# Optimization experiments

Measured on AMD Instinct MI355X. Metric: run time of the kernel, lower is better.

## Reference

```python
import jax, jax.numpy as jnp
import numpy as np

B, T, D, H = 2, 2048, 1024, 16
HD = D // H  # 64
SCALE = 1.0 / np.sqrt(D).astype(np.float32)  # module uses 1/sqrt(mod_dim), not head_dim


def setup_inputs() -> dict:
    key = jax.random.key(0)
    k1, k2, k3 = jax.random.split(key, 3)
    x = jax.random.normal(k1, (B, T, D), dtype=jnp.float32)
    W_attn = jax.random.normal(k2, (3 * D, D), dtype=jnp.float32) * 0.02
    W_out = jax.random.normal(k3, (D, D), dtype=jnp.float32) * 0.02
    return {"x": x, "W_attn": W_attn, "W_out": W_out}


def reference(x, W_attn, W_out):
    b, t, d = x.shape
    # qkv projection (Linear, no bias): x @ W^T
    qkv = jnp.einsum('btd,ed->bte', x, W_attn)  # [b, t, 3d]
    q, k, v = jnp.split(qkv, 3, axis=-1)
    # [b, h, t, hd]
    q = q.reshape(b, t, H, HD).transpose(0, 2, 1, 3)
    k = k.reshape(b, t, H, HD).transpose(0, 2, 1, 3)
    v = v.reshape(b, t, H, HD).transpose(0, 2, 1, 3)
    # raw scores, causal mask applied before scaling (scale*-inf == -inf, so
    # equivalent to the original mask-then-scale order)
    att = jnp.einsum('bhqd,bhkd->bhqk', q, k)
    causal = jnp.tril(jnp.ones((t, t), dtype=bool))
    att = jnp.where(causal[None, None], att * SCALE, -jnp.inf)
    att = jax.nn.softmax(att, axis=-1)
    z = jnp.einsum('bhqk,bhkd->bhqd', att, v)
    z = z.transpose(0, 2, 1, 3).reshape(b, t, d)
    return jnp.einsum('btd,od->bto', z, W_out)
```

## Files before the change

### kernel.cpp

```cpp
#include <hip/hip_runtime.h>
#include <cstddef>

typedef unsigned short u16;
typedef __attribute__((ext_vector_type(4))) float floatx4;
typedef __attribute__((ext_vector_type(8))) short short8;
typedef __attribute__((ext_vector_type(4))) unsigned int uintx4;

#define TT 2048
#define DD 1024
#define NH 16
#define ATT_SCALE (1.0f / 32.0f)

__device__ __forceinline__ u16 f2bf(float f) {
  unsigned u = __builtin_bit_cast(unsigned, f);
  u += 0x7fffu + ((u >> 16) & 1u);
  return (u16)(u >> 16);
}

__device__ __forceinline__ unsigned pack2(float a, float b) {
#if __has_builtin(__builtin_amdgcn_cvt_pk_bf16_f32)
  auto t = __builtin_amdgcn_cvt_pk_bf16_f32(a, b);
  return __builtin_bit_cast(unsigned, t);
#else
  unsigned ua = __builtin_bit_cast(unsigned, a);
  ua += 0x7fffu + ((ua >> 16) & 1u);
  unsigned ub = __builtin_bit_cast(unsigned, b);
  ub += 0x7fffu + ((ub >> 16) & 1u);
  return (ua >> 16) | (ub & 0xffff0000u);
#endif
}

__device__ __forceinline__ void g2l16(const u16* g, u16* l) {
#if __has_builtin(__builtin_amdgcn_global_load_lds)
  __builtin_amdgcn_global_load_lds(
      (const __attribute__((address_space(1))) unsigned int*)g,
      (__attribute__((address_space(3))) unsigned int*)l, 16, 0, 0);
#else
  *(int4*)l = *(const int4*)g;
#endif
}

__device__ __forceinline__ short8 scale_q(short8 q) {
  short8 r;
#pragma unroll
  for (int i = 0; i < 8; ++i) {
    float f = __builtin_bit_cast(float, ((unsigned)(u16)q[i]) << 16) * ATT_SCALE;
    r[i] = (short)f2bf(f);
  }
  return r;
}

__global__ __launch_bounds__(256) void cvt3_kernel(const float* __restrict__ a,
                                                   const float* __restrict__ b,
                                                   const float* __restrict__ c,
                                                   u16* __restrict__ out,
                                                   int na, int nb, int nc) {
  int i = blockIdx.x * 256 + threadIdx.x;
  const float* src;
  int j;
  if (i < na) { src = a; j = i; }
  else if (i < na + nb) { src = b; j = i - na; }
  else if (i < na + nb + nc) { src = c; j = i - na - nb; }
  else return;
  float4 v = ((const float4*)src)[j];
  ((ushort4*)out)[i] = make_ushort4(f2bf(v.x), f2bf(v.y), f2bf(v.z), f2bf(v.w));
}

template <int MODE, int BN>
__global__ __launch_bounds__(256) void gemm_bt(const u16* __restrict__ A,
                                               const u16* __restrict__ Bm,
                                               void* __restrict__ C,
                                               u16* __restrict__ vt,
                                               int M, int N, int K) {
  constexpr int NT = BN / 32;
  __shared__ u16 As[128 * 32];
  __shared__ u16 Bs[BN * 32];
  const int tid = threadIdx.x;
  const int lane = tid & 63;
  const int wave = tid >> 6;
  const int quad = lane >> 4;
  const int l16 = lane & 15;
  const int wm = (wave >> 1) * 64;
  const int wn = (wave & 1) * (BN / 2);
  const int m0 = blockIdx.x * 128;
  const int n0 = blockIdx.y * BN;

  const int srow = wave * 16 + (lane >> 2);
  const int scol = (lane & 3) * 8;
  const int sl = wave * 512 + lane * 8;

  floatx4 acc[4][NT] = {};

  for (int k0 = 0; k0 < K; k0 += 32) {
    __syncthreads();
    g2l16(&A[(size_t)(m0 + srow) * K + k0 + scol], &As[sl]);
    g2l16(&A[(size_t)(m0 + 64 + srow) * K + k0 + scol], &As[2048 + sl]);
    g2l16(&Bm[(size_t)(n0 + srow) * K + k0 + scol], &Bs[sl]);
    if (BN == 128)
      g2l16(&Bm[(size_t)(n0 + 64 + srow) * K + k0 + scol], &Bs[2048 + sl]);
    __syncthreads();

    short8 af[4];
#pragma unroll
    for (int mt = 0; mt < 4; ++mt)
      af[mt] = *(const short8*)&As[(wm + mt * 16 + l16) * 32 + quad * 8];
#pragma unroll
    for (int nt = 0; nt < NT; ++nt) {
      short8 bf = *(const short8*)&Bs[(wn + nt * 16 + l16) * 32 + quad * 8];
#pragma unroll
      for (int mt = 0; mt < 4; ++mt)
        acc[mt][nt] = __builtin_amdgcn_mfma_f32_16x16x32_bf16(af[mt], bf, acc[mt][nt], 0, 0, 0);
    }
  }

  if (MODE == 2 && n0 >= 2048) {
    const int bidx = m0 >> 11;
    const int tbase = (m0 & 2047) + wm;
#pragma unroll
    for (int mt = 0; mt < 4; ++mt)
#pragma unroll
      for (int nt = 0; nt < NT; ++nt) {
        int gn = n0 + wn + nt * 16 + l16;
        size_t vrow = (size_t)(bidx * 1024 + gn - 2048);
        int t = tbase + mt * 16 + quad * 4;
        uint2 val;
        val.x = pack2(acc[mt][nt][0], acc[mt][nt][1]);
        val.y = pack2(acc[mt][nt][2], acc[mt][nt][3]);
        *(uint2*)&vt[vrow * TT + t] = val;
      }
  } else {
    const int cw = (MODE == 2) ? 2048 : N;
#pragma unroll
    for (int mt = 0; mt < 4; ++mt)
#pragma unroll
      for (int nt = 0; nt < NT; ++nt)
#pragma unroll
        for (int r = 0; r < 4; ++r) {
          int gm = m0 + wm + mt * 16 + quad * 4 + r;
          int gn = n0 + wn + nt * 16 + l16;
          float v = acc[mt][nt][r];
          if (MODE >= 1)
            ((u16*)C)[(size_t)gm * cw + gn] = f2bf(v);
          else
            ((float*)C)[(size_t)gm * cw + gn] = v;
        }
  }
}

template <bool DIAG>
__device__ __forceinline__ void exp_pack(const floatx4* s, int kt0, int quad,
                                         int qr, float& ps, unsigned W[4][2]) {
#pragma unroll
  for (int nt = 0; nt < 4; ++nt) {
    float e[4];
#pragma unroll
    for (int r = 0; r < 4; ++r) {
      float v = __expf(s[nt][r]);
      if (DIAG) {
        int kk = kt0 + nt * 16 + quad * 4 + r;
        v = (kk <= qr) ? v : 0.f;
      }
      ps += v;
      e[r] = v;
    }
    W[nt][0] = pack2(e[0], e[1]);
    W[nt][1] = pack2(e[2], e[3]);
  }
}

__device__ __forceinline__ void pfrag(const unsigned W[4][2], int bpA, int bpB,
                                      int quad, short8& pa0, short8& pa1) {
  uintx4 a, b;
#pragma unroll
  for (int c = 0; c < 2; ++c) {
    unsigned x0 = (unsigned)__builtin_amdgcn_ds_bpermute(bpA, (int)W[0][c]);
    unsigned x1 = (unsigned)__builtin_amdgcn_ds_bpermute(bpA, (int)W[1][c]);
    unsigned y0 = (unsigned)__builtin_amdgcn_ds_bpermute(bpB, (int)W[0][c]);
    unsigned y1 = (unsigned)__builtin_amdgcn_ds_bpermute(bpB, (int)W[1][c]);
    a[c]     = (quad < 2) ? x0 : x1;
    a[2 + c] = (quad < 2) ? y0 : y1;
    unsigned u0 = (unsigned)__builtin_amdgcn_ds_bpermute(bpA, (int)W[2][c]);
    unsigned u1 = (unsigned)__builtin_amdgcn_ds_bpermute(bpA, (int)W[3][c]);
    unsigned t0 = (unsigned)__builtin_amdgcn_ds_bpermute(bpB, (int)W[2][c]);
    unsigned t1 = (unsigned)__builtin_amdgcn_ds_bpermute(bpB, (int)W[3][c]);
    b[c]     = (quad < 2) ? u0 : u1;
    b[2 + c] = (quad < 2) ? t0 : t1;
  }
  pa0 = __builtin_bit_cast(short8, a);
  pa1 = __builtin_bit_cast(short8, b);
}

__global__ __launch_bounds__(512, 4) void attn_flash6(const u16* __restrict__ qk,
                                                      const u16* __restrict__ vt,
                                                      u16* __restrict__ z) {
  __shared__ u16 Ks[2][64 * 64];
  __shared__ u16 Vs[2][64 * 64];

  const int tid = threadIdx.x;
  const int lane = tid & 63;
  const int wave = tid >> 6;
  const int qs = wave & 3;
  const int par = wave >> 2;
  const int quad = lane >> 4;
  const int l16 = lane & 15;

  const int p = blockIdx.x;
  const int qtA = p, qtB = 31 - p;
  const int bh = blockIdx.y;
  const int b = bh >> 4, h = bh & 15;

  const size_t bbase = (size_t)b * TT * 2048;
  const u16* qg = qk + bbase + h * 64;
  const u16* kg = qk + bbase + 1024 + h * 64;
  const u16* vtg = vt + (size_t)bh * 64 * TT;

  short8 qfA[2], qfB[2];
  {
    const size_t ra = (size_t)(qtA * 64 + qs * 16 + l16) * 2048;
    const size_t rb = (size_t)(qtB * 64 + qs * 16 + l16) * 2048;
    qfA[0] = scale_q(*(const short8*)&qg[ra + quad * 8]);
    qfA[1] = scale_q(*(const short8*)&qg[ra + 32 + quad * 8]);
    qfB[0] = scale_q(*(const short8*)&qg[rb + quad * 8]);
    qfB[1] = scale_q(*(const short8*)&qg[rb + 32 + quad * 8]);
  }

  floatx4 OA[4] = {}, OB[4] = {};
  float psA = 0.f, psB = 0.f;

  const int tsel = tid >> 8;
  const int t8 = tid & 255;
  const int str = t8 >> 2, sc = (t8 & 3) * 16;
  const int swr = (str & 7) << 3;

  const int nktB = qtB + 1;
  const int M = (nktB + 1) >> 1;
  const int qrA = qtA * 64 + qs * 16 + l16;
  const int qrB = qtB * 64 + qs * 16 + l16;

  const int sw = (l16 & 7) << 3;
  const int rc0 = (quad * 8) ^ sw;
  const int rc1 = (32 + quad * 8) ^ sw;
  const int bpA = ((((lane >> 4) & 1) << 5) | l16) << 2;
  const int bpB = bpA + 64;

  for (int m = 0; m < M; ++m) {
    const int kt = 2 * m + par;
    const int kt0 = kt * 64;
    __syncthreads();
    {
      const int kst = 2 * m + tsel;
      if (kst < nktB) {
        *(int4*)&Ks[tsel][str * 64 + (sc ^ swr)] =
            *(const int4*)&kg[(size_t)(kst * 64 + str) * 2048 + sc];
        *(int4*)&Ks[tsel][str * 64 + ((sc + 8) ^ swr)] =
            *(const int4*)&kg[(size_t)(kst * 64 + str) * 2048 + sc + 8];
        *(int4*)&Vs[tsel][str * 64 + (sc ^ swr)] =
            *(const int4*)&vtg[(size_t)str * TT + kst * 64 + sc];
        *(int4*)&Vs[tsel][str * 64 + ((sc + 8) ^ swr)] =
            *(const int4*)&vtg[(size_t)str * TT + kst * 64 + sc + 8];
      }
    }
    __syncthreads();

    if (kt < nktB) {
      floatx4 s[4];
      __builtin_amdgcn_s_setprio(1);
#pragma unroll
      for (int nt = 0; nt < 4; ++nt) {
        const int ro = (nt * 16 + l16) * 64;
        short8 k0 = *(const short8*)&Ks[par][ro + rc0];
        short8 k1 = *(const short8*)&Ks[par][ro + rc1];
        floatx4 zz = {0.f, 0.f, 0.f, 0.f};
        s[nt] = __builtin_amdgcn_mfma_f32_16x16x32_bf16(k0, qfB[0], zz, 0, 0, 0);
        s[nt] = __builtin_amdgcn_mfma_f32_16x16x32_bf16(k1, qfB[1], s[nt], 0, 0, 0);
      }
      __builtin_amdgcn_s_setprio(0);
      short8 pa0, pa1;
      {
        unsigned W[4][2];
        if (kt == qtB)
          exp_pack<true>(s, kt0, quad, qrB, psB, W);
        else
          exp_pack<false>(s, kt0, quad, qrB, psB, W);
        pfrag(W, bpA, bpB, quad, pa0, pa1);
      }
      __builtin_amdgcn_s_setprio(1);
#pragma unroll
      for (int nt = 0; nt < 4; ++nt) {
        const int ro = (nt * 16 + l16) * 64;
        short8 v0 = *(const short8*)&Vs[par][ro + rc0];
        short8 v1 = *(const short8*)&Vs[par][ro + rc1];
        OB[nt] = __builtin_amdgcn_mfma_f32_16x16x32_bf16(pa0, v0, OB[nt], 0, 0, 0);
        OB[nt] = __builtin_amdgcn_mfma_f32_16x16x32_bf16(pa1, v1, OB[nt], 0, 0, 0);
      }
      __builtin_amdgcn_s_setprio(0);

      if (kt <= qtA) {
        __builtin_amdgcn_s_setprio(1);
#pragma unroll
        for (int nt = 0; nt < 4; ++nt) {
          const int ro = (nt * 16 + l16) * 64;
          short8 k0 = *(const short8*)&Ks[par][ro + rc0];
          short8 k1 = *(const short8*)&Ks[par][ro + rc1];
          floatx4 zz = {0.f, 0.f, 0.f, 0.f};
          s[nt] = __builtin_amdgcn_mfma_f32_16x16x32_bf16(k0, qfA[0], zz, 0, 0, 0);
          s[nt] = __builtin_amdgcn_mfma_f32_16x16x32_bf16(k1, qfA[1], s[nt], 0, 0, 0);
        }
        __builtin_amdgcn_s_setprio(0);
        {
          unsigned W[4][2];
          if (kt == qtA)
            exp_pack<true>(s, kt0, quad, qrA, psA, W);
          else
            exp_pack<false>(s, kt0, quad, qrA, psA, W);
          pfrag(W, bpA, bpB, quad, pa0, pa1);
        }
        __builtin_amdgcn_s_setprio(1);
#pragma unroll
        for (int nt = 0; nt < 4; ++nt) {
          const int ro = (nt * 16 + l16) * 64;
          short8 v0 = *(const short8*)&Vs[par][ro + rc0];
          short8 v1 = *(const short8*)&Vs[par][ro + rc1];
          OA[nt] = __builtin_amdgcn_mfma_f32_16x16x32_bf16(pa0, v0, OA[nt], 0, 0, 0);
          OA[nt] = __builtin_amdgcn_mfma_f32_16x16x32_bf16(pa1, v1, OA[nt], 0, 0, 0);
        }
        __builtin_amdgcn_s_setprio(0);
      }
    }
  }

  psA += __shfl_xor(psA, 16);
  psA += __shfl_xor(psA, 32);
  psB += __shfl_xor(psB, 16);
  psB += __shfl_xor(psB, 32);

  float* red = (float*)Ks;
  float* lred = (float*)Vs;

  __syncthreads();
  if (par == 1) {
#pragma unroll
    for (int nt = 0; nt < 4; ++nt)
#pragma unroll
      for (int r = 0; r < 4; ++r)
        red[(qs * 16 + quad * 4 + r) * 64 + nt * 16 + l16] = OA[nt][r];
  }
  if (quad == 0) lred[par * 64 + qs * 16 + l16] = psA;
  __syncthreads();
  if (par == 0) {
#pragma unroll
    for (int r = 0; r < 4; ++r) {
      int row = qs * 16 + quad * 4 + r;
      float rl = 1.0f / (lred[row] + lred[64 + row]);
      int qa = qtA * 64 + row;
#pragma unroll
      for (int nt = 0; nt < 4; ++nt) {
        float o = OA[nt][r] + red[row * 64 + nt * 16 + l16];
        z[(size_t)(b * TT + qa) * DD + h * 64 + nt * 16 + l16] = f2bf(o * rl);
      }
    }
  }
  __syncthreads();
  if (par == 1) {
#pragma unroll
    for (int nt = 0; nt < 4; ++nt)
#pragma unroll
      for (int r = 0; r < 4; ++r)
        red[(qs * 16 + quad * 4 + r) * 64 + nt * 16 + l16] = OB[nt][r];
  }
  if (quad == 0) lred[par * 64 + qs * 16 + l16] = psB;
  __syncthreads();
  if (par == 0) {
#pragma unroll
    for (int r = 0; r < 4; ++r) {
      int row = qs * 16 + quad * 4 + r;
      float rl = 1.0f / (lred[row] + lred[64 + row]);
      int qb = qtB * 64 + row;
#pragma unroll
      for (int nt = 0; nt < 4; ++nt) {
        float o = OB[nt][r] + red[row * 64 + nt * 16 + l16];
        z[(size_t)(b * TT + qb) * DD + h * 64 + nt * 16 + l16] = f2bf(o * rl);
      }
    }
  }
}

extern "C" void kernel_launch(void* const* d_in, const int* in_sizes, int n_in,
                              void* d_out, int out_size, void* d_ws, size_t ws_size,
                              hipStream_t stream) {
  const float* x  = (const float*)d_in[0];
  const float* Wa = (const float*)d_in[1];
  const float* Wo = (const float*)d_in[2];
  float* out = (float*)d_out;

  u16* xb  = (u16*)d_ws;
  u16* Wab = xb  + (size_t)4096 * 1024;
  u16* Wob = Wab + (size_t)3072 * 1024;
  u16* qk  = Wob + (size_t)1024 * 1024;
  u16* z   = qk  + (size_t)4096 * 2048;
  u16* vt  = z   + (size_t)4096 * 1024;

  cvt3_kernel<<<8192, 256, 0, stream>>>(x, Wa, Wo, xb, 1048576, 786432, 262144);

  gemm_bt<2, 128><<<dim3(32, 24), 256, 0, stream>>>(xb, Wab, qk, vt, 4096, 3072, 1024);

  attn_flash6<<<dim3(16, 2 * NH), 512, 0, stream>>>(qk, vt, z);

  gemm_bt<0, 64><<<dim3(32, 16), 256, 0, stream>>>(z, Wob, out, nullptr, 4096, 1024, 1024);
}
```

Baseline: 180.0 us.

## Replace paired causal query tiles with one tile per block, heaviest first

The attention kernel no longer pairs query tile p with tile 31-p in one block for causal load balancing. Each block now handles a single query tile, launched in descending order so the longest tiles start first, doubling the grid to 32x32 blocks. Launch bounds rise to 8 blocks per CU to fit more resident blocks. This cuts per-block register use and gives finer scheduling granularity, but each K/V tile loaded into shared memory now serves only one query tile, and the extra blocks repeat setup and K/V loads.

```diff
diff --git a/kernel.cpp b/kernel.cpp
--- a/kernel.cpp
+++ b/kernel.cpp
@@ -190,7 +190,7 @@
   pa1 = __builtin_bit_cast(short8, b);
 }
 
-__global__ __launch_bounds__(512, 4) void attn_flash6(const u16* __restrict__ qk,
+__global__ __launch_bounds__(512, 8) void attn_flash7(const u16* __restrict__ qk,
                                                       const u16* __restrict__ vt,
                                                       u16* __restrict__ z) {
   __shared__ u16 Ks[2][64 * 64];
@@ -204,8 +204,7 @@
   const int quad = lane >> 4;
   const int l16 = lane & 15;
 
-  const int p = blockIdx.x;
-  const int qtA = p, qtB = 31 - p;
+  const int qt = 31 - blockIdx.x;
   const int bh = blockIdx.y;
   const int b = bh >> 4, h = bh & 15;
 
@@ -214,28 +213,24 @@
   const u16* kg = qk + bbase + 1024 + h * 64;
   const u16* vtg = vt + (size_t)bh * 64 * TT;
 
-  short8 qfA[2], qfB[2];
+  short8 qf[2];
   {
-    const size_t ra = (size_t)(qtA * 64 + qs * 16 + l16) * 2048;
-    const size_t rb = (size_t)(qtB * 64 + qs * 16 + l16) * 2048;
-    qfA[0] = scale_q(*(const short8*)&qg[ra + quad * 8]);
-    qfA[1] = scale_q(*(const short8*)&qg[ra + 32 + quad * 8]);
-    qfB[0] = scale_q(*(const short8*)&qg[rb + quad * 8]);
-    qfB[1] = scale_q(*(const short8*)&qg[rb + 32 + quad * 8]);
-  }
-
-  floatx4 OA[4] = {}, OB[4] = {};
-  float psA = 0.f, psB = 0.f;
+    const size_t ra = (size_t)(qt * 64 + qs * 16 + l16) * 2048;
+    qf[0] = scale_q(*(const short8*)&qg[ra + quad * 8]);
+    qf[1] = scale_q(*(const short8*)&qg[ra + 32 + quad * 8]);
+  }
+
+  floatx4 O[4] = {};
+  float ps = 0.f;
 
   const int tsel = tid >> 8;
   const int t8 = tid & 255;
   const int str = t8 >> 2, sc = (t8 & 3) * 16;
   const int swr = (str & 7) << 3;
 
-  const int nktB = qtB + 1;
-  const int M = (nktB + 1) >> 1;
-  const int qrA = qtA * 64 + qs * 16 + l16;
-  const int qrB = qtB * 64 + qs * 16 + l16;
+  const int nkt = qt + 1;
+  const int M = (nkt + 1) >> 1;
+  const int qr = qt * 64 + qs * 16 + l16;
 
   const int sw = (l16 & 7) << 3;
   const int rc0 = (quad * 8) ^ sw;
@@ -249,7 +244,7 @@
     __syncthreads();
     {
       const int kst = 2 * m + tsel;
-      if (kst < nktB) {
+      if (kst < nkt) {
         *(int4*)&Ks[tsel][str * 64 + (sc ^ swr)] =
             *(const int4*)&kg[(size_t)(kst * 64 + str) * 2048 + sc];
         *(int4*)&Ks[tsel][str * 64 + ((sc + 8) ^ swr)] =
@@ -262,7 +257,7 @@
     }
     __syncthreads();
 
-    if (kt < nktB) {
+    if (kt < nkt) {
       floatx4 s[4];
       __builtin_amdgcn_s_setprio(1);
 #pragma unroll
@@ -271,17 +266,17 @@
         short8 k0 = *(const short8*)&Ks[par][ro + rc0];
         short8 k1 = *(const short8*)&Ks[par][ro + rc1];
         floatx4 zz = {0.f, 0.f, 0.f, 0.f};
-        s[nt] = __builtin_amdgcn_mfma_f32_16x16x32_bf16(k0, qfB[0], zz, 0, 0, 0);
-        s[nt] = __builtin_amdgcn_mfma_f32_16x16x32_bf16(k1, qfB[1], s[nt], 0, 0, 0);
+        s[nt] = __builtin_amdgcn_mfma_f32_16x16x32_bf16(k0, qf[0], zz, 0, 0, 0);
+        s[nt] = __builtin_amdgcn_mfma_f32_16x16x32_bf16(k1, qf[1], s[nt], 0, 0, 0);
       }
       __builtin_amdgcn_s_setprio(0);
       short8 pa0, pa1;
       {
         unsigned W[4][2];
-        if (kt == qtB)
-          exp_pack<true>(s, kt0, quad, qrB, psB, W);
+        if (kt == qt)
+          exp_pack<true>(s, kt0, quad, qr, ps, W);
         else
-          exp_pack<false>(s, kt0, quad, qrB, psB, W);
+          exp_pack<false>(s, kt0, quad, qr, ps, W);
         pfrag(W, bpA, bpB, quad, pa0, pa1);
       }
       __builtin_amdgcn_s_setprio(1);
@@ -290,49 +285,15 @@
         const int ro = (nt * 16 + l16) * 64;
         short8 v0 = *(const short8*)&Vs[par][ro + rc0];
         short8 v1 = *(const short8*)&Vs[par][ro + rc1];
-        OB[nt] = __builtin_amdgcn_mfma_f32_16x16x32_bf16(pa0, v0, OB[nt], 0, 0, 0);
-        OB[nt] = __builtin_amdgcn_mfma_f32_16x16x32_bf16(pa1, v1, OB[nt], 0, 0, 0);
+        O[nt] = __builtin_amdgcn_mfma_f32_16x16x32_bf16(pa0, v0, O[nt], 0, 0, 0);
+        O[nt] = __builtin_amdgcn_mfma_f32_16x16x32_bf16(pa1, v1, O[nt], 0, 0, 0);
       }
       __builtin_amdgcn_s_setprio(0);
-
-      if (kt <= qtA) {
-        __builtin_amdgcn_s_setprio(1);
-#pragma unroll
-        for (int nt = 0; nt < 4; ++nt) {
-          const int ro = (nt * 16 + l16) * 64;
-          short8 k0 = *(const short8*)&Ks[par][ro + rc0];
-          short8 k1 = *(const short8*)&Ks[par][ro + rc1];
-          floatx4 zz = {0.f, 0.f, 0.f, 0.f};
-          s[nt] = __builtin_amdgcn_mfma_f32_16x16x32_bf16(k0, qfA[0], zz, 0, 0, 0);
-          s[nt] = __builtin_amdgcn_mfma_f32_16x16x32_bf16(k1, qfA[1], s[nt], 0, 0, 0);
-        }
-        __builtin_amdgcn_s_setprio(0);
-        {
-          unsigned W[4][2];
-          if (kt == qtA)
-            exp_pack<true>(s, kt0, quad, qrA, psA, W);
-          else
-            exp_pack<false>(s, kt0, quad, qrA, psA, W);
-          pfrag(W, bpA, bpB, quad, pa0, pa1);
-        }
-        __builtin_amdgcn_s_setprio(1);
-#pragma unroll
-        for (int nt = 0; nt < 4; ++nt) {
-          const int ro = (nt * 16 + l16) * 64;
-          short8 v0 = *(const short8*)&Vs[par][ro + rc0];
-          short8 v1 = *(const short8*)&Vs[par][ro + rc1];
-          OA[nt] = __builtin_amdgcn_mfma_f32_16x16x32_bf16(pa0, v0, OA[nt], 0, 0, 0);
-          OA[nt] = __builtin_amdgcn_mfma_f32_16x16x32_bf16(pa1, v1, OA[nt], 0, 0, 0);
-        }
-        __builtin_amdgcn_s_setprio(0);
-      }
-    }
-  }
-
-  psA += __shfl_xor(psA, 16);
-  psA += __shfl_xor(psA, 32);
-  psB += __shfl_xor(psB, 16);
-  psB += __shfl_xor(psB, 32);
+    }
+  }
+
+  ps += __shfl_xor(ps, 16);
+  ps += __shfl_xor(ps, 32);
 
   float* red = (float*)Ks;
   float* lred = (float*)Vs;
@@ -343,43 +304,20 @@
     for (int nt = 0; nt < 4; ++nt)
 #pragma unroll
       for (int r = 0; r < 4; ++r)
-        red[(qs * 16 + quad * 4 + r) * 64 + nt * 16 + l16] = OA[nt][r];
-  }
-  if (quad == 0) lred[par * 64 + qs * 16 + l16] = psA;
+        red[(qs * 16 + quad * 4 + r) * 64 + nt * 16 + l16] = O[nt][r];
+  }
+  if (quad == 0) lred[par * 64 + qs * 16 + l16] = ps;
   __syncthreads();
   if (par == 0) {
 #pragma unroll
     for (int r = 0; r < 4; ++r) {
       int row = qs * 16 + quad * 4 + r;
       float rl = 1.0f / (lred[row] + lred[64 + row]);
-      int qa = qtA * 64 + row;
+      int qa = qt * 64 + row;
 #pragma unroll
       for (int nt = 0; nt < 4; ++nt) {
-        float o = OA[nt][r] + red[row * 64 + nt * 16 + l16];
+        float o = O[nt][r] + red[row * 64 + nt * 16 + l16];
         z[(size_t)(b * TT + qa) * DD + h * 64 + nt * 16 + l16] = f2bf(o * rl);
-      }
-    }
-  }
-  __syncthreads();
-  if (par == 1) {
-#pragma unroll
-    for (int nt = 0; nt < 4; ++nt)
-#pragma unroll
-      for (int r = 0; r < 4; ++r)
-        red[(qs * 16 + quad * 4 + r) * 64 + nt * 16 + l16] = OB[nt][r];
-  }
-  if (quad == 0) lred[par * 64 + qs * 16 + l16] = psB;
-  __syncthreads();
-  if (par == 0) {
-#pragma unroll
-    for (int r = 0; r < 4; ++r) {
-      int row = qs * 16 + quad * 4 + r;
-      float rl = 1.0f / (lred[row] + lred[64 + row]);
-      int qb = qtB * 64 + row;
-#pragma unroll
-      for (int nt = 0; nt < 4; ++nt) {
-        float o = OB[nt][r] + red[row * 64 + nt * 16 + l16];
-        z[(size_t)(b * TT + qb) * DD + h * 64 + nt * 16 + l16] = f2bf(o * rl);
       }
     }
   }
@@ -404,7 +342,7 @@
 
   gemm_bt<2, 128><<<dim3(32, 24), 256, 0, stream>>>(xb, Wab, qk, vt, 4096, 3072, 1024);
 
-  attn_flash6<<<dim3(16, 2 * NH), 512, 0, stream>>>(qk, vt, z);
+  attn_flash7<<<dim3(32, 2 * NH), 512, 0, stream>>>(qk, vt, z);
 
   gemm_bt<0, 64><<<dim3(32, 16), 256, 0, stream>>>(z, Wob, out, nullptr, 4096, 1024, 1024);
 }
```

New measurement: 220.0 us. +22.2%, slower.

## Double GEMM K-tile to 64 with XOR-swizzled LDS layout

Applied to the files above, without the earlier changes.

The GEMM kernels now stage a 64-wide K slice per iteration instead of 32, which halves the number of barrier pairs and loop iterations. Each thread loads rows of 8 bf16 into LDS with an XOR swizzle on the column chunk, and the MFMA fragment reads apply the same swizzle to avoid LDS bank conflicts on the wider 128-byte rows. LDS use per block doubles, which may reduce occupancy.

```diff
diff --git a/kernel.cpp b/kernel.cpp
--- a/kernel.cpp
+++ b/kernel.cpp
@@ -67,14 +67,15 @@
 }
 
 template <int MODE, int BN>
-__global__ __launch_bounds__(256) void gemm_bt(const u16* __restrict__ A,
-                                               const u16* __restrict__ Bm,
-                                               void* __restrict__ C,
-                                               u16* __restrict__ vt,
-                                               int M, int N, int K) {
+__global__ __launch_bounds__(256) void gemm_bt64(const u16* __restrict__ A,
+                                                 const u16* __restrict__ Bm,
+                                                 void* __restrict__ C,
+                                                 u16* __restrict__ vt,
+                                                 int M, int N, int K) {
   constexpr int NT = BN / 32;
-  __shared__ u16 As[128 * 32];
-  __shared__ u16 Bs[BN * 32];
+  constexpr int BOPS = BN / 32;
+  __shared__ u16 As[128 * 64];
+  __shared__ u16 Bs[BN * 64];
   const int tid = threadIdx.x;
   const int lane = tid & 63;
   const int wave = tid >> 6;
@@ -85,31 +86,39 @@
   const int m0 = blockIdx.x * 128;
   const int n0 = blockIdx.y * BN;
 
-  const int srow = wave * 16 + (lane >> 2);
-  const int scol = (lane & 3) * 8;
-  const int sl = wave * 512 + lane * 8;
+  const int srow = tid >> 3;
+  const int scol = ((tid & 7) ^ (srow & 7)) * 8;
+  const int sdst = tid * 8;
+
+  const int sw8 = l16 & 7;
 
   floatx4 acc[4][NT] = {};
 
-  for (int k0 = 0; k0 < K; k0 += 32) {
+  for (int k0 = 0; k0 < K; k0 += 64) {
     __syncthreads();
-    g2l16(&A[(size_t)(m0 + srow) * K + k0 + scol], &As[sl]);
-    g2l16(&A[(size_t)(m0 + 64 + srow) * K + k0 + scol], &As[2048 + sl]);
-    g2l16(&Bm[(size_t)(n0 + srow) * K + k0 + scol], &Bs[sl]);
-    if (BN == 128)
-      g2l16(&Bm[(size_t)(n0 + 64 + srow) * K + k0 + scol], &Bs[2048 + sl]);
+#pragma unroll
+    for (int o = 0; o < 4; ++o)
+      g2l16(&A[(size_t)(m0 + o * 32 + srow) * K + k0 + scol], &As[o * 2048 + sdst]);
+#pragma unroll
+    for (int o = 0; o < BOPS; ++o)
+      g2l16(&Bm[(size_t)(n0 + o * 32 + srow) * K + k0 + scol], &Bs[o * 2048 + sdst]);
     __syncthreads();
 
-    short8 af[4];
-#pragma unroll
-    for (int mt = 0; mt < 4; ++mt)
-      af[mt] = *(const short8*)&As[(wm + mt * 16 + l16) * 32 + quad * 8];
-#pragma unroll
-    for (int nt = 0; nt < NT; ++nt) {
-      short8 bf = *(const short8*)&Bs[(wn + nt * 16 + l16) * 32 + quad * 8];
+#pragma unroll
+    for (int kk = 0; kk < 2; ++kk) {
+      short8 af[4];
 #pragma unroll
       for (int mt = 0; mt < 4; ++mt)
-        acc[mt][nt] = __builtin_amdgcn_mfma_f32_16x16x32_bf16(af[mt], bf, acc[mt][nt], 0, 0, 0);
+        af[mt] = *(const short8*)&As[(wm + mt * 16 + l16) * 64 +
+                                     (((kk << 2) | quad) ^ sw8) * 8];
+#pragma unroll
+      for (int nt = 0; nt < NT; ++nt) {
+        short8 bf = *(const short8*)&Bs[(wn + nt * 16 + l16) * 64 +
+                                        (((kk << 2) | quad) ^ sw8) * 8];
+#pragma unroll
+        for (int mt = 0; mt < 4; ++mt)
+          acc[mt][nt] = __builtin_amdgcn_mfma_f32_16x16x32_bf16(af[mt], bf, acc[mt][nt], 0, 0, 0);
+      }
     }
   }
 
@@ -402,9 +411,9 @@
 
   cvt3_kernel<<<8192, 256, 0, stream>>>(x, Wa, Wo, xb, 1048576, 786432, 262144);
 
-  gemm_bt<2, 128><<<dim3(32, 24), 256, 0, stream>>>(xb, Wab, qk, vt, 4096, 3072, 1024);
+  gemm_bt64<2, 128><<<dim3(32, 24), 256, 0, stream>>>(xb, Wab, qk, vt, 4096, 3072, 1024);
 
   attn_flash6<<<dim3(16, 2 * NH), 512, 0, stream>>>(qk, vt, z);
 
-  gemm_bt<0, 64><<<dim3(32, 16), 256, 0, stream>>>(z, Wob, out, nullptr, 4096, 1024, 1024);
-}
+  gemm_bt64<0, 64><<<dim3(32, 16), 256, 0, stream>>>(z, Wob, out, nullptr, 4096, 1024, 1024);
+}
```

Result: faster. 174.3 us (-3.2%).
